# Performance work log

Hardware: AMD Instinct MI355X
Metric: run time of the kernel (lower is better)

The kernel has to match this reference:

```python
import jax, jax.numpy as jnp
import numpy as np

S = 16          # spatial_size (adaptive pool output per dim)
EPS = 1e-8      # torch.cosine_similarity eps

def _avg_pool3d(x, s):
    # exact adaptive avg pool when D,H,W divisible by s
    B, C, D, H, W = x.shape
    kd, kh, kw = D // s, H // s, W // s
    x = x.reshape(B, C, s, kd, s, kh, s, kw)
    return x.mean(axis=(3, 5, 7))  # (B, C, s, s, s)

def _flatten_rows(x):
    # (B,C,s,s,s) -> (B*s^3, C), matching view+transpose+flatten
    B, C = x.shape[0], x.shape[1]
    return x.reshape(B, C, -1).transpose(0, 2, 1).reshape(-1, C)

def _cos_sim_matrix(a):
    # pairwise cosine similarity via normalize + GEMM
    norms = jnp.maximum(jnp.linalg.norm(a, axis=-1, keepdims=True), EPS)
    an = a / norms
    return an @ an.T  # (N, N)

def setup_inputs() -> dict:
    key = jax.random.key(0)
    k1, k2 = jax.random.split(key)
    shape = (2, 32, 64, 64, 64)
    p1 = jax.random.normal(k1, shape, dtype=jnp.float32)
    p2 = jax.random.normal(k2, shape, dtype=jnp.float32)
    return {"p1": p1, "p2": p2}

def reference(p1, p2):
    aa = _flatten_rows(_avg_pool3d(p1, S))  # (N, C), N = B*S^3
    bb = _flatten_rows(_avg_pool3d(p2, S))
    sim_a = _cos_sim_matrix(aa)
    sim_b = _cos_sim_matrix(bb)
    return jnp.mean((sim_a - sim_b) ** 2)  # MSELoss
```

## Files before the change

### kernel.cpp

```cpp
#include <hip/hip_runtime.h>
#include <hip/hip_bf16.h>


#define HW   4096
#define DHW  262144
#define NROW 8192
#define C    32

__device__ __forceinline__ float4 f4add(const float4 a, const float4 b) {
    return make_float4(a.x + b.x, a.y + b.y, a.z + b.z, a.w + b.w);
}

__global__ __launch_bounds__(256) void pool_kernel(
    const float* __restrict__ p1, const float* __restrict__ p2,
    float* __restrict__ Pa, float* __restrict__ Pb, float* __restrict__ G)
{
    const int tid = threadIdx.x;
    const int bid = blockIdx.x;

    if (bid == 0) {
        #pragma unroll
        for (int i = 0; i < 13; ++i) {
            const int idx = tid + i * 256;
            if (idx < 3136) G[idx] = 0.f;
        }
    }

    const int zp  = bid & 15;
    const int c   = (bid >> 4) & 31;
    const int b   = (bid >> 9) & 1;
    const int arr = bid >> 10;

    const float* __restrict__ src = arr ? p2 : p1;
    float* __restrict__ dst       = arr ? Pb : Pa;

    const float4* __restrict__ base = reinterpret_cast<const float4*>(
        src + (size_t)(b * C + c) * DHW + (size_t)(zp * 4) * HW);

    const int lane = tid & 63;
    const int w    = tid >> 6;

    __shared__ float pool[256];

    float4 v[8], acc[4];
    #pragma unroll
    for (int p = 0; p < 8; ++p) v[p] = base[p * 256 + tid];
    #pragma unroll
    for (int j = 0; j < 4; ++j) acc[j] = f4add(v[j], v[j + 4]);
    #pragma unroll
    for (int p = 0; p < 8; ++p) v[p] = base[(p + 8) * 256 + tid];
    #pragma unroll
    for (int j = 0; j < 4; ++j) acc[j] = f4add(acc[j], f4add(v[j], v[j + 4]));

    #pragma unroll
    for (int j = 0; j < 4; ++j) {
        float s = (acc[j].x + acc[j].y) + (acc[j].z + acc[j].w);
        s += __shfl_xor(s, 16);
        s += __shfl_xor(s, 32);
        const int yp = (4 * j + w) & 15;
        if (lane < 16) pool[yp * 16 + lane] = s * (1.0f / 64.0f);
    }
    __syncthreads();

    const int n = b * 4096 + zp * 256 + tid;
    dst[(size_t)n * C + c] = pool[tid];
}

__global__ __launch_bounds__(256) void gram_kernel(
    const float* __restrict__ Pa, const float* __restrict__ Pb,
    float* __restrict__ G,
    float* __restrict__ out)
{
    const int tid = threadIdx.x;
    const int k  = tid >> 3;
    const int l4 = (tid & 7) * 4;

    __shared__ float As[32 * C];
    __shared__ float Bs[32 * C];

    const int r = blockIdx.x * 32;
    float4 va = reinterpret_cast<const float4*>(Pa + (size_t)r * C)[tid];
    float4 vb = reinterpret_cast<const float4*>(Pb + (size_t)r * C)[tid];

    float ssa = va.x*va.x + va.y*va.y + va.z*va.z + va.w*va.w;
    float ssb = vb.x*vb.x + vb.y*vb.y + vb.z*vb.z + vb.w*vb.w;
    ssa += __shfl_xor(ssa, 1); ssa += __shfl_xor(ssa, 2); ssa += __shfl_xor(ssa, 4);
    ssb += __shfl_xor(ssb, 1); ssb += __shfl_xor(ssb, 2); ssb += __shfl_xor(ssb, 4);
    const float inva = 1.0f / fmaxf(sqrtf(ssa), 1e-8f);
    const float invb = 1.0f / fmaxf(sqrtf(ssb), 1e-8f);
    va.x *= inva; va.y *= inva; va.z *= inva; va.w *= inva;
    vb.x *= invb; vb.y *= invb; vb.z *= invb; vb.w *= invb;

    reinterpret_cast<float4*>(As)[tid] = va;
    reinterpret_cast<float4*>(Bs)[tid] = vb;
    __syncthreads();

    float gaa[4] = {0.f, 0.f, 0.f, 0.f};
    float gab[4] = {0.f, 0.f, 0.f, 0.f};
    float gbb[4] = {0.f, 0.f, 0.f, 0.f};

    #pragma unroll
    for (int i = 0; i < 32; ++i) {
        const float a_k = As[i * C + k];
        const float b_k = Bs[i * C + k];
        const float4 a_l = *reinterpret_cast<const float4*>(&As[i * C + l4]);
        const float4 b_l = *reinterpret_cast<const float4*>(&Bs[i * C + l4]);
        gaa[0] += a_k * a_l.x;  gaa[1] += a_k * a_l.y;
        gaa[2] += a_k * a_l.z;  gaa[3] += a_k * a_l.w;
        gab[0] += a_k * b_l.x;  gab[1] += a_k * b_l.y;
        gab[2] += a_k * b_l.z;  gab[3] += a_k * b_l.w;
        gbb[0] += b_k * b_l.x;  gbb[1] += b_k * b_l.y;
        gbb[2] += b_k * b_l.z;  gbb[3] += b_k * b_l.w;
    }

    #pragma unroll
    for (int j = 0; j < 4; ++j) {
        atomicAdd(&G[k * C + l4 + j],        gaa[j]);
        atomicAdd(&G[1024 + k * C + l4 + j], gab[j]);
        atomicAdd(&G[2048 + k * C + l4 + j], gbb[j]);
    }

    __syncthreads();
    __shared__ int last_flag;
    if (tid == 0) {
        __threadfence();
        const unsigned t = __hip_atomic_fetch_add(
            reinterpret_cast<unsigned*>(G + 3072), 1u,
            __ATOMIC_ACQ_REL, __HIP_MEMORY_SCOPE_AGENT);
        last_flag = (t == (unsigned)(gridDim.x - 1));
    }
    __syncthreads();
    if (!last_flag) return;

    float vv = 0.f;
    #pragma unroll
    for (int e0 = 0; e0 < 1024; e0 += 256) {
        const int e = e0 + tid;
        const float gA = __hip_atomic_load(G + e,        __ATOMIC_RELAXED, __HIP_MEMORY_SCOPE_AGENT);
        const float gX = __hip_atomic_load(G + 1024 + e, __ATOMIC_RELAXED, __HIP_MEMORY_SCOPE_AGENT);
        const float gB = __hip_atomic_load(G + 2048 + e, __ATOMIC_RELAXED, __HIP_MEMORY_SCOPE_AGENT);
        vv += gA * gA + gB * gB - 2.f * gX * gX;
    }
    vv += __shfl_xor(vv, 1);  vv += __shfl_xor(vv, 2);  vv += __shfl_xor(vv, 4);
    vv += __shfl_xor(vv, 8);  vv += __shfl_xor(vv, 16); vv += __shfl_xor(vv, 32);

    __shared__ float red[4];
    if ((tid & 63) == 0) red[tid >> 6] = vv;
    __syncthreads();
    if (tid == 0)
        out[0] = (red[0] + red[1] + red[2] + red[3]) * (1.0f / ((float)NROW * (float)NROW));
}

extern "C" void kernel_launch(void* const* d_in, const int* in_sizes, int n_in,
                              void* d_out, int out_size, void* d_ws, size_t ws_size,
                              hipStream_t stream) {
    const float* p1 = (const float*)d_in[0];
    const float* p2 = (const float*)d_in[1];
    float* out = (float*)d_out;

    float* Pa = (float*)d_ws;
    float* Pb = Pa + (size_t)NROW * C;
    float* G  = Pb + (size_t)NROW * C;

    pool_kernel<<<2048, 256, 0, stream>>>(p1, p2, Pa, Pb, G);
    gram_kernel<<<256, 256, 0, stream>>>(Pa, Pb, G, out);
}
```

Measured before the change: 180.6 us.

## Fuse pooling and Gram accumulation into one kernel with nontemporal loads

Merges the pooling and Gram kernels into one kernel. Each block pools one (b,z,y) strip of 16 rows across all 32 channels for both inputs, normalizes the rows in shared memory, and atomically accumulates its partial Gram matrices. This removes the intermediate pooled-row buffers, one kernel launch, and the transposed scattered stores. It also switches to nontemporal vector loads. The global zeroing moves to a hipMemsetAsync. The new load pattern reads 16-byte pieces strided by row and plane, which is less contiguous than before and may hurt DRAM efficiency. There are also twice as many blocks issuing global atomics.

Measured after the change: 194.3 us. 1.08x slower.

```diff
diff --git a/kernel.cpp b/kernel.cpp
--- a/kernel.cpp
+++ b/kernel.cpp
@@ -7,134 +7,109 @@
 #define NROW 8192
 #define C    32
 
-__device__ __forceinline__ float4 f4add(const float4 a, const float4 b) {
-    return make_float4(a.x + b.x, a.y + b.y, a.z + b.z, a.w + b.w);
+typedef float fx4 __attribute__((ext_vector_type(4)));
+
+__device__ __forceinline__ float hsum4(const fx4 v) {
+    return (v.x + v.y) + (v.z + v.w);
 }
 
-__global__ __launch_bounds__(256) void pool_kernel(
+__global__ __launch_bounds__(512) void fused_kernel(
     const float* __restrict__ p1, const float* __restrict__ p2,
-    float* __restrict__ Pa, float* __restrict__ Pb, float* __restrict__ G)
-{
-    const int tid = threadIdx.x;
-    const int bid = blockIdx.x;
-
-    if (bid == 0) {
-        #pragma unroll
-        for (int i = 0; i < 13; ++i) {
-            const int idx = tid + i * 256;
-            if (idx < 3136) G[idx] = 0.f;
-        }
-    }
-
-    const int zp  = bid & 15;
-    const int c   = (bid >> 4) & 31;
-    const int b   = (bid >> 9) & 1;
-    const int arr = bid >> 10;
-
-    const float* __restrict__ src = arr ? p2 : p1;
-    float* __restrict__ dst       = arr ? Pb : Pa;
-
-    const float4* __restrict__ base = reinterpret_cast<const float4*>(
-        src + (size_t)(b * C + c) * DHW + (size_t)(zp * 4) * HW);
-
-    const int lane = tid & 63;
-    const int w    = tid >> 6;
-
-    __shared__ float pool[256];
-
-    float4 v[8], acc[4];
-    #pragma unroll
-    for (int p = 0; p < 8; ++p) v[p] = base[p * 256 + tid];
-    #pragma unroll
-    for (int j = 0; j < 4; ++j) acc[j] = f4add(v[j], v[j + 4]);
-    #pragma unroll
-    for (int p = 0; p < 8; ++p) v[p] = base[(p + 8) * 256 + tid];
-    #pragma unroll
-    for (int j = 0; j < 4; ++j) acc[j] = f4add(acc[j], f4add(v[j], v[j + 4]));
-
-    #pragma unroll
-    for (int j = 0; j < 4; ++j) {
-        float s = (acc[j].x + acc[j].y) + (acc[j].z + acc[j].w);
-        s += __shfl_xor(s, 16);
-        s += __shfl_xor(s, 32);
-        const int yp = (4 * j + w) & 15;
-        if (lane < 16) pool[yp * 16 + lane] = s * (1.0f / 64.0f);
-    }
-    __syncthreads();
-
-    const int n = b * 4096 + zp * 256 + tid;
-    dst[(size_t)n * C + c] = pool[tid];
-}
-
-__global__ __launch_bounds__(256) void gram_kernel(
-    const float* __restrict__ Pa, const float* __restrict__ Pb,
     float* __restrict__ G,
     float* __restrict__ out)
 {
     const int tid = threadIdx.x;
-    const int k  = tid >> 3;
-    const int l4 = (tid & 7) * 4;
+    const int bid = blockIdx.x;
+    const int y = bid & 15;
+    const int z = (bid >> 4) & 15;
+    const int b = bid >> 8;
 
-    __shared__ float As[32 * C];
-    __shared__ float Bs[32 * C];
+    const int inp = tid >> 8;
+    const int t   = tid & 255;
+    const int x   = t & 15;
+    const int c0  = t >> 4;
 
-    const int r = blockIdx.x * 32;
-    float4 va = reinterpret_cast<const float4*>(Pa + (size_t)r * C)[tid];
-    float4 vb = reinterpret_cast<const float4*>(Pb + (size_t)r * C)[tid];
+    __shared__ __align__(16) float Rows[2][16][C];
+    __shared__ float normsq[2][16];
 
-    float ssa = va.x*va.x + va.y*va.y + va.z*va.z + va.w*va.w;
-    float ssb = vb.x*vb.x + vb.y*vb.y + vb.z*vb.z + vb.w*vb.w;
-    ssa += __shfl_xor(ssa, 1); ssa += __shfl_xor(ssa, 2); ssa += __shfl_xor(ssa, 4);
-    ssb += __shfl_xor(ssb, 1); ssb += __shfl_xor(ssb, 2); ssb += __shfl_xor(ssb, 4);
-    const float inva = 1.0f / fmaxf(sqrtf(ssa), 1e-8f);
-    const float invb = 1.0f / fmaxf(sqrtf(ssb), 1e-8f);
-    va.x *= inva; va.y *= inva; va.z *= inva; va.w *= inva;
-    vb.x *= invb; vb.y *= invb; vb.z *= invb; vb.w *= invb;
+    if (tid < 32) normsq[tid >> 4][tid & 15] = 0.f;
 
-    reinterpret_cast<float4*>(As)[tid] = va;
-    reinterpret_cast<float4*>(Bs)[tid] = vb;
+    const float* __restrict__ src = inp ? p2 : p1;
+    const size_t off = (size_t)(4 * z) * HW + (size_t)(4 * y) * 64 + 4 * x;
+    const fx4* __restrict__ base0 =
+        reinterpret_cast<const fx4*>(src + (size_t)(b * C + c0) * DHW + off);
+    const fx4* __restrict__ base1 =
+        reinterpret_cast<const fx4*>(src + (size_t)(b * C + c0 + 16) * DHW + off);
+
+    float s0[4] = {0.f, 0.f, 0.f, 0.f};
+    float s1[4] = {0.f, 0.f, 0.f, 0.f};
+    #pragma unroll
+    for (int dy = 0; dy < 4; ++dy) {
+        const fx4 a0 = __builtin_nontemporal_load(base0 + dy * 16 + 0 * 1024);
+        const fx4 a1 = __builtin_nontemporal_load(base0 + dy * 16 + 1 * 1024);
+        const fx4 a2 = __builtin_nontemporal_load(base0 + dy * 16 + 2 * 1024);
+        const fx4 a3 = __builtin_nontemporal_load(base0 + dy * 16 + 3 * 1024);
+        const fx4 b0 = __builtin_nontemporal_load(base1 + dy * 16 + 0 * 1024);
+        const fx4 b1 = __builtin_nontemporal_load(base1 + dy * 16 + 1 * 1024);
+        const fx4 b2 = __builtin_nontemporal_load(base1 + dy * 16 + 2 * 1024);
+        const fx4 b3 = __builtin_nontemporal_load(base1 + dy * 16 + 3 * 1024);
+        s0[0] += hsum4(a0); s0[1] += hsum4(a1); s0[2] += hsum4(a2); s0[3] += hsum4(a3);
+        s1[0] += hsum4(b0); s1[1] += hsum4(b1); s1[2] += hsum4(b2); s1[3] += hsum4(b3);
+    }
+    const float pooled0 = ((s0[0] + s0[1]) + (s0[2] + s0[3])) * (1.0f / 64.0f);
+    const float pooled1 = ((s1[0] + s1[1]) + (s1[2] + s1[3])) * (1.0f / 64.0f);
+
+    __syncthreads();
+    atomicAdd(&normsq[inp][x], pooled0 * pooled0 + pooled1 * pooled1);
     __syncthreads();
 
-    float gaa[4] = {0.f, 0.f, 0.f, 0.f};
-    float gab[4] = {0.f, 0.f, 0.f, 0.f};
-    float gbb[4] = {0.f, 0.f, 0.f, 0.f};
+    const float inv = 1.0f / fmaxf(sqrtf(normsq[inp][x]), 1e-8f);
+    Rows[inp][x][c0]      = pooled0 * inv;
+    Rows[inp][x][c0 + 16] = pooled1 * inv;
+    __syncthreads();
 
-    #pragma unroll
-    for (int i = 0; i < 32; ++i) {
-        const float a_k = As[i * C + k];
-        const float b_k = Bs[i * C + k];
-        const float4 a_l = *reinterpret_cast<const float4*>(&As[i * C + l4]);
-        const float4 b_l = *reinterpret_cast<const float4*>(&Bs[i * C + l4]);
-        gaa[0] += a_k * a_l.x;  gaa[1] += a_k * a_l.y;
-        gaa[2] += a_k * a_l.z;  gaa[3] += a_k * a_l.w;
-        gab[0] += a_k * b_l.x;  gab[1] += a_k * b_l.y;
-        gab[2] += a_k * b_l.z;  gab[3] += a_k * b_l.w;
-        gbb[0] += b_k * b_l.x;  gbb[1] += b_k * b_l.y;
-        gbb[2] += b_k * b_l.z;  gbb[3] += b_k * b_l.w;
-    }
-
-    #pragma unroll
-    for (int j = 0; j < 4; ++j) {
-        atomicAdd(&G[k * C + l4 + j],        gaa[j]);
-        atomicAdd(&G[1024 + k * C + l4 + j], gab[j]);
-        atomicAdd(&G[2048 + k * C + l4 + j], gbb[j]);
+    if (tid < 256) {
+        const int k  = tid >> 3;
+        const int l4 = (tid & 7) * 4;
+        float gaa[4] = {0.f, 0.f, 0.f, 0.f};
+        float gab[4] = {0.f, 0.f, 0.f, 0.f};
+        float gbb[4] = {0.f, 0.f, 0.f, 0.f};
+        #pragma unroll
+        for (int i = 0; i < 16; ++i) {
+            const float a_k = Rows[0][i][k];
+            const float b_k = Rows[1][i][k];
+            const fx4 a_l = *reinterpret_cast<const fx4*>(&Rows[0][i][l4]);
+            const fx4 b_l = *reinterpret_cast<const fx4*>(&Rows[1][i][l4]);
+            gaa[0] += a_k * a_l.x;  gaa[1] += a_k * a_l.y;
+            gaa[2] += a_k * a_l.z;  gaa[3] += a_k * a_l.w;
+            gab[0] += a_k * b_l.x;  gab[1] += a_k * b_l.y;
+            gab[2] += a_k * b_l.z;  gab[3] += a_k * b_l.w;
+            gbb[0] += b_k * b_l.x;  gbb[1] += b_k * b_l.y;
+            gbb[2] += b_k * b_l.z;  gbb[3] += b_k * b_l.w;
+        }
+        #pragma unroll
+        for (int j = 0; j < 4; ++j) {
+            atomicAdd(&G[k * C + l4 + j],        gaa[j]);
+            atomicAdd(&G[1024 + k * C + l4 + j], gab[j]);
+            atomicAdd(&G[2048 + k * C + l4 + j], gbb[j]);
+        }
     }
 
     __syncthreads();
     __shared__ int last_flag;
     if (tid == 0) {
         __threadfence();
-        const unsigned t = __hip_atomic_fetch_add(
+        const unsigned tk = __hip_atomic_fetch_add(
             reinterpret_cast<unsigned*>(G + 3072), 1u,
             __ATOMIC_ACQ_REL, __HIP_MEMORY_SCOPE_AGENT);
-        last_flag = (t == (unsigned)(gridDim.x - 1));
+        last_flag = (tk == (unsigned)(gridDim.x - 1));
     }
     __syncthreads();
     if (!last_flag) return;
 
     float vv = 0.f;
     #pragma unroll
-    for (int e0 = 0; e0 < 1024; e0 += 256) {
+    for (int e0 = 0; e0 < 1024; e0 += 512) {
         const int e = e0 + tid;
         const float gA = __hip_atomic_load(G + e,        __ATOMIC_RELAXED, __HIP_MEMORY_SCOPE_AGENT);
         const float gX = __hip_atomic_load(G + 1024 + e, __ATOMIC_RELAXED, __HIP_MEMORY_SCOPE_AGENT);
@@ -144,11 +119,15 @@
     vv += __shfl_xor(vv, 1);  vv += __shfl_xor(vv, 2);  vv += __shfl_xor(vv, 4);
     vv += __shfl_xor(vv, 8);  vv += __shfl_xor(vv, 16); vv += __shfl_xor(vv, 32);
 
-    __shared__ float red[4];
+    __shared__ float red[8];
     if ((tid & 63) == 0) red[tid >> 6] = vv;
     __syncthreads();
-    if (tid == 0)
-        out[0] = (red[0] + red[1] + red[2] + red[3]) * (1.0f / ((float)NROW * (float)NROW));
+    if (tid == 0) {
+        float tot = 0.f;
+        #pragma unroll
+        for (int i = 0; i < 8; ++i) tot += red[i];
+        out[0] = tot * (1.0f / ((float)NROW * (float)NROW));
+    }
 }
 
 extern "C" void kernel_launch(void* const* d_in, const int* in_sizes, int n_in,
@@ -158,10 +137,8 @@
     const float* p2 = (const float*)d_in[1];
     float* out = (float*)d_out;
 
-    float* Pa = (float*)d_ws;
-    float* Pb = Pa + (size_t)NROW * C;
-    float* G  = Pb + (size_t)NROW * C;
+    float* G = (float*)d_ws;
 
-    pool_kernel<<<2048, 256, 0, stream>>>(p1, p2, Pa, Pb, G);
-    gram_kernel<<<256, 256, 0, stream>>>(Pa, Pb, G, out);
+    (void)hipMemsetAsync(G, 0, 3136 * sizeof(float), stream);
+    fused_kernel<<<512, 512, 0, stream>>>(p1, p2, G, out);
 }
```
